# Optimization experiments

Measured on AMD Instinct MI355X. Metric: run time of the kernel, lower is better.

Reference implementation:

```python
import jax, jax.numpy as jnp
import numpy as np

# Complete binary tree: B trees, L leaves each, processed level-synchronously.
B, L, IN_DIM, MEM = 64, 1024, 300, 256


def setup_inputs() -> dict:
    key = jax.random.key(0)
    ks = jax.random.split(key, 6)
    s = 0.05
    embs = jax.random.normal(ks[0], (B, L, IN_DIM), dtype=jnp.float32)
    # Leaf module: c = cx(x); h = sigmoid(ox(x)) * tanh(c)
    Wcx = jax.random.normal(ks[1], (MEM, IN_DIM), dtype=jnp.float32) * s
    bcx = jnp.zeros((MEM,), jnp.float32)
    Wox = jax.random.normal(ks[2], (MEM, IN_DIM), dtype=jnp.float32) * s
    box = jnp.zeros((MEM,), jnp.float32)
    # Composer: 4 gates (i, lf, rf, u), each gate = Linear(lh) + Linear(rh).
    # Stacked: Wl/Wr have shape [4, MEM, MEM]; biases [4, MEM].
    Wl = jax.random.normal(ks[3], (4, MEM, MEM), dtype=jnp.float32) * s
    bl = jnp.zeros((4, MEM), jnp.float32)
    Wr = jax.random.normal(ks[4], (4, MEM, MEM), dtype=jnp.float32) * s
    br = jnp.zeros((4, MEM), jnp.float32)
    return dict(embs=embs, Wcx=Wcx, bcx=bcx, Wox=Wox, box=box,
                Wl=Wl, bl=bl, Wr=Wr, br=br)


def reference(embs, Wcx, bcx, Wox, box, Wl, bl, Wr, br):
    # Leaf module (BinaryTreeLeafModule.forward), vectorized over all leaves.
    c = jnp.einsum('blx,mx->blm', embs, Wcx) + bcx          # [B, L, MEM]
    o = jax.nn.sigmoid(jnp.einsum('blx,mx->blm', embs, Wox) + box)
    h = o * jnp.tanh(c)

    bias = bl + br                                          # [4, MEM]
    n = c.shape[1]
    while n > 1:  # log2(L) levels, static unrolled loop
        lc, rc = c[:, 0::2], c[:, 1::2]                     # [B, n/2, MEM]
        lh, rh = h[:, 0::2], h[:, 1::2]
        # All 4 gate pre-activations fused: [B, n/2, 4, MEM]
        g = (jnp.einsum('bnm,gom->bngo', lh, Wl)
             + jnp.einsum('bnm,gom->bngo', rh, Wr) + bias)
        i = jax.nn.sigmoid(g[..., 0, :])
        lf = jax.nn.sigmoid(g[..., 1, :])
        rf = jax.nn.sigmoid(g[..., 2, :])
        u = jnp.tanh(g[..., 3, :])
        c = i * u + lf * lc + rf * rc                       # composer cell
        h = jnp.tanh(c)                                     # gate_output=False path
        n //= 2

    # Root state (tree.state = (c, h)); stacked as [2, B, MEM]
    return jnp.stack([c[:, 0], h[:, 0]])
```

## Files before the change

### kernel.cpp

```cpp
#include <hip/hip_runtime.h>
#include <hip/hip_bf16.h>


typedef __attribute__((ext_vector_type(8))) short bf16x8;
typedef __attribute__((ext_vector_type(4))) float f32x4;

__device__ __forceinline__ float fsig(float x)  { return 1.f / (1.f + __expf(-x)); }
__device__ __forceinline__ float ftanh(float x) { return 1.f - 2.f / (__expf(2.f * x) + 1.f); }
__device__ __forceinline__ ushort f2bf(float x) {
    __hip_bfloat16 b = __float2bfloat16(x);
    return *reinterpret_cast<ushort*>(&b);
}

__device__ __forceinline__ void gld_lds16(const void* g, void* l) {
    __builtin_amdgcn_global_load_lds((const __attribute__((address_space(1))) void*)g,
                                     (__attribute__((address_space(3))) void*)l, 16, 0, 0);
}

__global__ void prep(const float* __restrict__ Wl,  const float* __restrict__ Wr,
                     const float* __restrict__ bl,  const float* __restrict__ br,
                     const float* __restrict__ Wcx, const float* __restrict__ Wox,
                     const float* __restrict__ bcx, const float* __restrict__ box,
                     const float* __restrict__ embs,
                     ushort* __restrict__ Wb2, ushort* __restrict__ WbL,
                     float* __restrict__ bp2, float* __restrict__ bpL,
                     ushort* __restrict__ embsB)
{
    const int gid = blockIdx.x * 256 + threadIdx.x;
    for (int i = gid; i < 524288; i += 262144) {
        int e = i & 7, slot = (i >> 3) & 3, o = (i >> 5) & 255;
        int g = (i >> 13) & 3, t = i >> 15;
        int q = slot ^ ((o >> 1) & 3);
        int k = t * 32 + q * 8 + e;
        float v = (k < 256) ? Wl[(g * 256 + o) * 256 + k]
                            : Wr[(g * 256 + o) * 256 + (k - 256)];
        Wb2[i] = f2bf(v);
    }
    if (gid < 163840) {
        int e = gid & 7, slot = (gid >> 3) & 3, o = (gid >> 5) & 255;
        int g = (gid >> 13) & 1, t = gid >> 14;
        int q = slot ^ ((o >> 1) & 3);
        int k = t * 32 + q * 8 + e;
        float v = 0.f;
        if (k < 300) v = g ? Wox[o * 300 + k] : Wcx[o * 300 + k];
        WbL[gid] = f2bf(v);
    }
    if (gid < 1024) bp2[gid] = bl[gid] + br[gid];
    if (gid < 512) {
        int g = gid >> 8, o = gid & 255;
        bpL[gid] = g ? box[o] : bcx[o];
    }
    for (int i = gid; i < 65536 * 80; i += 262144) {
        int row = i / 80;
        int k = (i - row * 80) * 4;
        float4 v = make_float4(0.f, 0.f, 0.f, 0.f);
        if (k < 300) v = *(const float4*)(embs + (size_t)row * 300 + k);
        ushort4 o4;
        o4.x = f2bf(v.x); o4.y = f2bf(v.y); o4.z = f2bf(v.z); o4.w = f2bf(v.w);
        *(ushort4*)(embsB + (size_t)row * 320 + k) = o4;
    }
}


template<int NG, int HALVES, int MODE>
__global__ __launch_bounds__(256, 3)
void mfma_gemm(const ushort* __restrict__ A,
               const ushort* __restrict__ Wb,
               const float* __restrict__ bp,
               const float* __restrict__ Cprev,
               float* __restrict__ c_out,
               ushort* __restrict__ h_out,
               int M)
{
    constexpr int K = HALVES * 32;
    constexpr int OW = 128 / NG;
    __shared__ __align__(16) ushort As[3][512 * 8];
    __shared__ __align__(16) ushort Bs[3][512 * 8];

    const int tid = threadIdx.x;
    const int wid = tid >> 6, ln = tid & 63;
    const int lq = ln >> 4, lr = ln & 15;
    const int wm = wid >> 1, wn = wid & 1;
    const int rowBlk = blockIdx.x * 128;
    const int o0 = blockIdx.y * OW;

    f32x4 acc[4][4];
#pragma unroll
    for (int m = 0; m < 4; ++m)
#pragma unroll
        for (int f = 0; f < 4; ++f) acc[m][f] = f32x4{0.f, 0.f, 0.f, 0.f};

    const int ar0 = tid >> 2,  as0 = tid & 3;
    const int ar1 = ar0 + 64;
    const int aq0 = (as0 - ((ar0 >> 1) & 3)) & 3;
    const int aq1 = (as0 - ((ar1 >> 1) & 3)) & 3;
    const ushort* aP0 = A + (size_t)min(rowBlk + ar0, M - 1) * K + aq0 * 8;
    const ushort* aP1 = A + (size_t)min(rowBlk + ar1, M - 1) * K + aq1 * 8;
    const int bj0 = tid >> 2,        bs0 = tid & 3;
    const int bj1 = (tid + 256) >> 2;
    const int bg0 = bj0 / OW, bo0 = o0 + (bj0 & (OW - 1));
    const int bg1 = bj1 / OW, bo1 = o0 + (bj1 & (OW - 1));
    const ushort* bP0 = Wb + ((size_t)bg0 * 1024 + bo0 * 4 + bs0) * 8;
    const ushort* bP1 = Wb + ((size_t)bg1 * 1024 + bo1 * 4 + bs0) * 8;
    constexpr size_t BSTR = (size_t)NG * 1024 * 8;

    const int aSw = (lq + ((lr >> 1) & 3)) & 3;
    const int bSw = lq ^ ((lr >> 1) & 3);
    int aOff[4];
#pragma unroll
    for (int m = 0; m < 4; ++m)
        aOff[m] = ((wm * 64 + m * 16 + lr) * 4 + aSw) * 8;
    int bOff[4];
#pragma unroll
    for (int f = 0; f < 4; ++f)
        bOff[f] = ((f * 32 + wn * 16 + lr) * 4 + bSw) * 8;

    gld_lds16(aP0, &As[0][tid * 8]);
    gld_lds16(aP1, &As[0][(tid + 256) * 8]);
    gld_lds16(bP0, &Bs[0][tid * 8]);
    gld_lds16(bP1, &Bs[0][(tid + 256) * 8]);
    gld_lds16(aP0 + 32, &As[1][tid * 8]);
    gld_lds16(aP1 + 32, &As[1][(tid + 256) * 8]);
    gld_lds16(bP0 + BSTR, &Bs[1][tid * 8]);
    gld_lds16(bP1 + BSTR, &Bs[1][(tid + 256) * 8]);
    asm volatile("s_waitcnt vmcnt(4)" ::: "memory");
    __builtin_amdgcn_s_barrier();
    __builtin_amdgcn_sched_barrier(0);

#pragma unroll
    for (int h = 0; h < HALVES; ++h) {
        const ushort* Ac = &As[h % 3][0];
        const ushort* Bc = &Bs[h % 3][0];
        if (h + 2 < HALVES) {
            ushort* An = &As[(h + 2) % 3][0];
            ushort* Bn = &Bs[(h + 2) % 3][0];
            gld_lds16(aP0 + (size_t)(h + 2) * 32, An + tid * 8);
            gld_lds16(aP1 + (size_t)(h + 2) * 32, An + (tid + 256) * 8);
            gld_lds16(bP0 + (size_t)(h + 2) * BSTR, Bn + tid * 8);
            gld_lds16(bP1 + (size_t)(h + 2) * BSTR, Bn + (tid + 256) * 8);
        }
        bf16x8 a[4];
#pragma unroll
        for (int m = 0; m < 4; ++m)
            a[m] = *(const bf16x8*)(Ac + aOff[m]);
#pragma unroll
        for (int f = 0; f < 4; ++f) {
            bf16x8 b = *(const bf16x8*)(Bc + bOff[f]);
#pragma unroll
            for (int m = 0; m < 4; ++m)
                acc[m][f] = __builtin_amdgcn_mfma_f32_16x16x32_bf16(a[m], b, acc[m][f], 0, 0, 0);
        }
        if (h + 1 < HALVES) {
            if (h + 2 < HALVES) asm volatile("s_waitcnt vmcnt(4)" ::: "memory");
            else                asm volatile("s_waitcnt vmcnt(0)" ::: "memory");
            __builtin_amdgcn_s_barrier();
            __builtin_amdgcn_sched_barrier(0);
        }
    }

#pragma unroll
    for (int m = 0; m < 4; ++m) {
        const int row0 = rowBlk + wm * 64 + m * 16 + lq * 4;
        if constexpr (MODE == 0) {
#pragma unroll
            for (int ob = 0; ob < 2; ++ob) {
                const int col = o0 + ob * 32 + wn * 16 + lr;
                const float bc = bp[col], bo = bp[256 + col];
#pragma unroll
                for (int j = 0; j < 4; ++j) {
                    int row = row0 + j;
                    if (row < M) {
                        float cv = acc[m][ob][j] + bc;
                        float ov = acc[m][2 + ob][j] + bo;
                        c_out[(size_t)row * 256 + col] = cv;
                        h_out[(size_t)row * 256 + col] = f2bf(fsig(ov) * ftanh(cv));
                    }
                }
            }
        } else {
            const int col = o0 + wn * 16 + lr;
            const float bi  = bp[col],       blf = bp[256 + col];
            const float brf = bp[512 + col], bu  = bp[768 + col];
#pragma unroll
            for (int j = 0; j < 4; ++j) {
                int row = row0 + j;
                if (row < M) {
                    float gi = fsig(acc[m][0][j] + bi);
                    float lf = fsig(acc[m][1][j] + blf);
                    float rf = fsig(acc[m][2][j] + brf);
                    float gu = ftanh(acc[m][3][j] + bu);
                    float lc = Cprev[(size_t)row * 512 + col];
                    float rc = Cprev[(size_t)row * 512 + 256 + col];
                    float cv = gi * gu + lf * lc + rf * rc;
                    c_out[(size_t)row * 256 + col] = cv;
                    h_out[(size_t)row * 256 + col] = f2bf(ftanh(cv));
                }
            }
        }
    }
}


__global__ __launch_bounds__(512, 1)
void tail_lstm(const ushort* __restrict__ hin,
               const float* __restrict__ cin,
               const ushort* __restrict__ Wb,
               const float* __restrict__ bp,
               float* __restrict__ dout)
{
    __shared__ __align__(16) ushort H0[64 * 256];
    __shared__ __align__(16) ushort H1[32 * 256];
    __shared__ __align__(16) float  C0[64 * 256];
    __shared__ __align__(16) float  C1[32 * 256];

    const int b = blockIdx.x;
    const int tid = threadIdx.x;
    const int wid = tid >> 6, ln = tid & 63;
    const int lq = ln >> 4, lr = ln & 15;

    for (int ct = tid; ct < 2048; ct += 512) {
        int pr = ct >> 5, pc = ct & 31;
        bf16x8 v = *(const bf16x8*)(hin + ((size_t)(b * 64 + pr) * 256 + pc * 8));
        *(bf16x8*)&H0[pr * 256 + ((pc ^ ((pr >> 1) & 7)) * 8)] = v;
    }
    for (int i = tid; i < 4096; i += 512)
        *(float4*)&C0[i * 4] = *(const float4*)(cin + (size_t)b * 64 * 256 + i * 4);
    __syncthreads();

    int o_[2], sl_[2];
    const ushort* bB[2];
#pragma unroll
    for (int of = 0; of < 2; ++of) {
        o_[of] = wid * 32 + of * 16 + lr;
        sl_[of] = lq ^ ((o_[of] >> 1) & 3);
        bB[of] = Wb + (size_t)(o_[of] * 4 + sl_[of]) * 8;
    }
    const float bi0  = bp[o_[0]],       blf0 = bp[256 + o_[0]];
    const float brf0 = bp[512 + o_[0]], bu0  = bp[768 + o_[0]];
    const float bi1  = bp[o_[1]],       blf1 = bp[256 + o_[1]];
    const float brf1 = bp[512 + o_[1]], bu1  = bp[768 + o_[1]];

    {
        f32x4 acc[2][2][4];
#pragma unroll
        for (int m = 0; m < 2; ++m)
#pragma unroll
            for (int of = 0; of < 2; ++of)
#pragma unroll
                for (int g = 0; g < 4; ++g) acc[m][of][g] = f32x4{0.f, 0.f, 0.f, 0.f};

        bf16x8 b0[2][4], b1[2][4], a0[2], a1[2];
#pragma unroll
        for (int of = 0; of < 2; ++of)
#pragma unroll
            for (int g = 0; g < 4; ++g)
                b0[of][g] = *(const bf16x8*)(bB[of] + (size_t)g * 8192);
#pragma unroll
        for (int m = 0; m < 2; ++m) {
            int pr = 32 * m + 2 * lr, pc = lq;
            a0[m] = *(const bf16x8*)&H0[pr * 256 + ((pc ^ ((pr >> 1) & 7)) * 8)];
        }

#pragma unroll 1
        for (int ks = 0; ks < 16; ks += 2) {
            if (ks + 1 < 16) {
#pragma unroll
                for (int of = 0; of < 2; ++of)
#pragma unroll
                    for (int g = 0; g < 4; ++g)
                        b1[of][g] = *(const bf16x8*)(bB[of] + (size_t)((ks + 1) * 4 + g) * 8192);
#pragma unroll
                for (int m = 0; m < 2; ++m) {
                    int pr = 32 * m + 2 * lr + ((ks + 1) >> 3), pc = lq + ((ks + 1) & 7) * 4;
                    a1[m] = *(const bf16x8*)&H0[pr * 256 + ((pc ^ ((pr >> 1) & 7)) * 8)];
                }
            }
#pragma unroll
            for (int m = 0; m < 2; ++m)
#pragma unroll
                for (int of = 0; of < 2; ++of)
#pragma unroll
                    for (int g = 0; g < 4; ++g)
                        acc[m][of][g] = __builtin_amdgcn_mfma_f32_16x16x32_bf16(a0[m], b0[of][g], acc[m][of][g], 0, 0, 0);
            if (ks + 2 < 16) {
#pragma unroll
                for (int of = 0; of < 2; ++of)
#pragma unroll
                    for (int g = 0; g < 4; ++g)
                        b0[of][g] = *(const bf16x8*)(bB[of] + (size_t)((ks + 2) * 4 + g) * 8192);
#pragma unroll
                for (int m = 0; m < 2; ++m) {
                    int pr = 32 * m + 2 * lr + ((ks + 2) >> 3), pc = lq + ((ks + 2) & 7) * 4;
                    a0[m] = *(const bf16x8*)&H0[pr * 256 + ((pc ^ ((pr >> 1) & 7)) * 8)];
                }
            }
#pragma unroll
            for (int m = 0; m < 2; ++m)
#pragma unroll
                for (int of = 0; of < 2; ++of)
#pragma unroll
                    for (int g = 0; g < 4; ++g)
                        acc[m][of][g] = __builtin_amdgcn_mfma_f32_16x16x32_bf16(a1[m], b1[of][g], acc[m][of][g], 0, 0, 0);
        }

#pragma unroll
        for (int m = 0; m < 2; ++m)
#pragma unroll
        for (int of = 0; of < 2; ++of) {
            const int col = o_[of];
            const float vbi  = of ? bi1 : bi0,   vblf = of ? blf1 : blf0;
            const float vbrf = of ? brf1 : brf0, vbu  = of ? bu1 : bu0;
#pragma unroll
            for (int j = 0; j < 4; ++j) {
                int row = m * 16 + lq * 4 + j;
                float gi = fsig(acc[m][of][0][j] + vbi);
                float lf = fsig(acc[m][of][1][j] + vblf);
                float rf = fsig(acc[m][of][2][j] + vbrf);
                float gu = ftanh(acc[m][of][3][j] + vbu);
                float lc = C0[(2 * row) * 256 + col];
                float rc = C0[(2 * row + 1) * 256 + col];
                float cv = gi * gu + lf * lc + rf * rc;
                float hv = ftanh(cv);
                C1[row * 256 + col] = cv;
                H1[row * 256 + (((col >> 3) ^ ((row >> 1) & 7)) * 8) + (col & 7)] = f2bf(hv);
            }
        }
        __syncthreads();
    }

#pragma unroll 1
    for (int lvl = 1; lvl < 6; ++lvl) {
        const int npo = 32 >> lvl;
        const ushort* Hin = (lvl & 1) ? H1 : H0;
        ushort*       Hout = (lvl & 1) ? H0 : H1;
        const float*  Cin = (lvl & 1) ? C1 : C0;
        float*        Cout = (lvl & 1) ? C0 : C1;

        f32x4 acc[2][4];
#pragma unroll
        for (int of = 0; of < 2; ++of)
#pragma unroll
            for (int g = 0; g < 4; ++g) acc[of][g] = f32x4{0.f, 0.f, 0.f, 0.f};

        bf16x8 b0[2][4], b1[2][4], a0, a1;
#pragma unroll
        for (int of = 0; of < 2; ++of)
#pragma unroll
            for (int g = 0; g < 4; ++g)
                b0[of][g] = *(const bf16x8*)(bB[of] + (size_t)g * 8192);
        {
            int pr = 2 * lr, pc = lq;
            a0 = *(const bf16x8*)&Hin[pr * 256 + ((pc ^ ((pr >> 1) & 7)) * 8)];
        }

#pragma unroll 1
        for (int ks = 0; ks < 16; ks += 2) {
            if (ks + 1 < 16) {
#pragma unroll
                for (int of = 0; of < 2; ++of)
#pragma unroll
                    for (int g = 0; g < 4; ++g)
                        b1[of][g] = *(const bf16x8*)(bB[of] + (size_t)((ks + 1) * 4 + g) * 8192);
                int pr = 2 * lr + ((ks + 1) >> 3), pc = lq + ((ks + 1) & 7) * 4;
                a1 = *(const bf16x8*)&Hin[pr * 256 + ((pc ^ ((pr >> 1) & 7)) * 8)];
            }
#pragma unroll
            for (int of = 0; of < 2; ++of)
#pragma unroll
                for (int g = 0; g < 4; ++g)
                    acc[of][g] = __builtin_amdgcn_mfma_f32_16x16x32_bf16(a0, b0[of][g], acc[of][g], 0, 0, 0);
            if (ks + 2 < 16) {
#pragma unroll
                for (int of = 0; of < 2; ++of)
#pragma unroll
                    for (int g = 0; g < 4; ++g)
                        b0[of][g] = *(const bf16x8*)(bB[of] + (size_t)((ks + 2) * 4 + g) * 8192);
                int pr = 2 * lr + ((ks + 2) >> 3), pc = lq + ((ks + 2) & 7) * 4;
                a0 = *(const bf16x8*)&Hin[pr * 256 + ((pc ^ ((pr >> 1) & 7)) * 8)];
            }
#pragma unroll
            for (int of = 0; of < 2; ++of)
#pragma unroll
                for (int g = 0; g < 4; ++g)
                    acc[of][g] = __builtin_amdgcn_mfma_f32_16x16x32_bf16(a1, b1[of][g], acc[of][g], 0, 0, 0);
        }

#pragma unroll
        for (int of = 0; of < 2; ++of) {
            const int col = o_[of];
            const float vbi  = of ? bi1 : bi0,   vblf = of ? blf1 : blf0;
            const float vbrf = of ? brf1 : brf0, vbu  = of ? bu1 : bu0;
#pragma unroll
            for (int j = 0; j < 4; ++j) {
                int row = lq * 4 + j;
                if (row < npo) {
                    float gi = fsig(acc[of][0][j] + vbi);
                    float lf = fsig(acc[of][1][j] + vblf);
                    float rf = fsig(acc[of][2][j] + vbrf);
                    float gu = ftanh(acc[of][3][j] + vbu);
                    float lc = Cin[(2 * row) * 256 + col];
                    float rc = Cin[(2 * row + 1) * 256 + col];
                    float cv = gi * gu + lf * lc + rf * rc;
                    float hv = ftanh(cv);
                    if (lvl == 5) {
                        dout[b * 256 + col] = cv;
                        dout[16384 + b * 256 + col] = hv;
                    } else {
                        Cout[row * 256 + col] = cv;
                        Hout[row * 256 + (((col >> 3) ^ ((row >> 1) & 7)) * 8) + (col & 7)] = f2bf(hv);
                    }
                }
            }
        }
        __syncthreads();
    }
}


extern "C" void kernel_launch(void* const* d_in, const int* in_sizes, int n_in,
                              void* d_out, int out_size, void* d_ws, size_t ws_size,
                              hipStream_t stream)
{
    const float* embs = (const float*)d_in[0];
    const float* Wcx  = (const float*)d_in[1];
    const float* bcx  = (const float*)d_in[2];
    const float* Wox  = (const float*)d_in[3];
    const float* box  = (const float*)d_in[4];
    const float* Wl   = (const float*)d_in[5];
    const float* bl   = (const float*)d_in[6];
    const float* Wr   = (const float*)d_in[7];
    const float* br   = (const float*)d_in[8];

    char* p = (char*)d_ws;
    ushort* Wb2 = (ushort*)p;  p += (size_t)524288 * 2;
    ushort* WbL = (ushort*)p;  p += (size_t)163840 * 2;
    float*  bp2 = (float*)p;   p += 1024 * 4;
    float*  bpL = (float*)p;   p += 512 * 4;
    float*  c0  = (float*)p;   p += (size_t)65536 * 256 * 4;
    ushort* h0  = (ushort*)p;  p += (size_t)65536 * 256 * 2;
    char* X = p;
    ushort* embsB = (ushort*)X;
    float*  cA = (float*)X;
    ushort* hA = (ushort*)(X + (size_t)32768 * 256 * 4);
    float*  cB = (float*)(X + (size_t)48 * 1024 * 1024);
    ushort* hB = (ushort*)(X + (size_t)64 * 1024 * 1024);

    prep<<<1024, 256, 0, stream>>>(Wl, Wr, bl, br, Wcx, Wox, bcx, box, embs,
                                   Wb2, WbL, bp2, bpL, embsB);

    mfma_gemm<2, 10, 0><<<dim3(512, 4), 256, 0, stream>>>(
        embsB, WbL, bpL, nullptr, c0, h0, 65536);

    mfma_gemm<4, 16, 1><<<dim3(256, 8), 256, 0, stream>>>(
        h0, Wb2, bp2, c0, cA, hA, 32768);
    mfma_gemm<4, 16, 1><<<dim3(128, 8), 256, 0, stream>>>(
        hA, Wb2, bp2, cA, cB, hB, 16384);
    mfma_gemm<4, 16, 1><<<dim3(64, 8), 256, 0, stream>>>(
        hB, Wb2, bp2, cB, cA, hA, 8192);
    mfma_gemm<4, 16, 1><<<dim3(32, 8), 256, 0, stream>>>(
        hA, Wb2, bp2, cA, cB, hB, 4096);

    tail_lstm<<<64, 512, 0, stream>>>(
        hB, cB, Wb2, bp2, (float*)d_out);
}
```

Baseline: 270.4 us.

## Store LSTM cell state in fp16 and simplify GEMM LDS pipeline

The intermediate cell-state buffers c between tree levels are now stored as fp16 instead of fp32. This halves the global memory traffic for writing and reading c in the leaf GEMM, the level GEMMs and the tail kernel, and shrinks the workspace layout. The GEMM moves from a 3-stage LDS ring with manual vmcnt waits to a 2-stage double buffer guarded by __syncthreads, and launch bounds rise to 4 blocks per CU. The tail kernel also drops its LDS staging of the first level and reads h and c straight from global memory. The risks are fp16 rounding error in c across ten levels and weaker latency hiding from the shallower prefetch.

```diff
diff --git a/kernel.cpp b/kernel.cpp
--- a/kernel.cpp
+++ b/kernel.cpp
@@ -1,5 +1,6 @@
 #include <hip/hip_runtime.h>
 #include <hip/hip_bf16.h>
+#include <hip/hip_fp16.h>
 
 
 typedef __attribute__((ext_vector_type(8))) short bf16x8;
@@ -63,19 +64,19 @@
 
 
 template<int NG, int HALVES, int MODE>
-__global__ __launch_bounds__(256, 3)
+__global__ __launch_bounds__(256, 4)
 void mfma_gemm(const ushort* __restrict__ A,
                const ushort* __restrict__ Wb,
                const float* __restrict__ bp,
-               const float* __restrict__ Cprev,
-               float* __restrict__ c_out,
+               const __half* __restrict__ Cprev,
+               __half* __restrict__ c_out,
                ushort* __restrict__ h_out,
                int M)
 {
     constexpr int K = HALVES * 32;
     constexpr int OW = 128 / NG;
-    __shared__ __align__(16) ushort As[3][512 * 8];
-    __shared__ __align__(16) ushort Bs[3][512 * 8];
+    __shared__ __align__(16) ushort As[2][512 * 8];
+    __shared__ __align__(16) ushort Bs[2][512 * 8];
 
     const int tid = threadIdx.x;
     const int wid = tid >> 6, ln = tid & 63;
@@ -119,42 +120,27 @@
     gld_lds16(aP1, &As[0][(tid + 256) * 8]);
     gld_lds16(bP0, &Bs[0][tid * 8]);
     gld_lds16(bP1, &Bs[0][(tid + 256) * 8]);
-    gld_lds16(aP0 + 32, &As[1][tid * 8]);
-    gld_lds16(aP1 + 32, &As[1][(tid + 256) * 8]);
-    gld_lds16(bP0 + BSTR, &Bs[1][tid * 8]);
-    gld_lds16(bP1 + BSTR, &Bs[1][(tid + 256) * 8]);
-    asm volatile("s_waitcnt vmcnt(4)" ::: "memory");
-    __builtin_amdgcn_s_barrier();
-    __builtin_amdgcn_sched_barrier(0);
 
 #pragma unroll
     for (int h = 0; h < HALVES; ++h) {
-        const ushort* Ac = &As[h % 3][0];
-        const ushort* Bc = &Bs[h % 3][0];
-        if (h + 2 < HALVES) {
-            ushort* An = &As[(h + 2) % 3][0];
-            ushort* Bn = &Bs[(h + 2) % 3][0];
-            gld_lds16(aP0 + (size_t)(h + 2) * 32, An + tid * 8);
-            gld_lds16(aP1 + (size_t)(h + 2) * 32, An + (tid + 256) * 8);
-            gld_lds16(bP0 + (size_t)(h + 2) * BSTR, Bn + tid * 8);
-            gld_lds16(bP1 + (size_t)(h + 2) * BSTR, Bn + (tid + 256) * 8);
+        __syncthreads();
+        const int cur = h & 1;
+        if (h + 1 < HALVES) {
+            gld_lds16(aP0 + (size_t)(h + 1) * 32, &As[cur ^ 1][tid * 8]);
+            gld_lds16(aP1 + (size_t)(h + 1) * 32, &As[cur ^ 1][(tid + 256) * 8]);
+            gld_lds16(bP0 + (size_t)(h + 1) * BSTR, &Bs[cur ^ 1][tid * 8]);
+            gld_lds16(bP1 + (size_t)(h + 1) * BSTR, &Bs[cur ^ 1][(tid + 256) * 8]);
         }
         bf16x8 a[4];
 #pragma unroll
         for (int m = 0; m < 4; ++m)
-            a[m] = *(const bf16x8*)(Ac + aOff[m]);
+            a[m] = *(const bf16x8*)&As[cur][aOff[m]];
 #pragma unroll
         for (int f = 0; f < 4; ++f) {
-            bf16x8 b = *(const bf16x8*)(Bc + bOff[f]);
+            bf16x8 b = *(const bf16x8*)&Bs[cur][bOff[f]];
 #pragma unroll
             for (int m = 0; m < 4; ++m)
                 acc[m][f] = __builtin_amdgcn_mfma_f32_16x16x32_bf16(a[m], b, acc[m][f], 0, 0, 0);
-        }
-        if (h + 1 < HALVES) {
-            if (h + 2 < HALVES) asm volatile("s_waitcnt vmcnt(4)" ::: "memory");
-            else                asm volatile("s_waitcnt vmcnt(0)" ::: "memory");
-            __builtin_amdgcn_s_barrier();
-            __builtin_amdgcn_sched_barrier(0);
         }
     }
 
@@ -172,7 +158,7 @@
                     if (row < M) {
                         float cv = acc[m][ob][j] + bc;
                         float ov = acc[m][2 + ob][j] + bo;
-                        c_out[(size_t)row * 256 + col] = cv;
+                        c_out[(size_t)row * 256 + col] = __float2half(cv);
                         h_out[(size_t)row * 256 + col] = f2bf(fsig(ov) * ftanh(cv));
                     }
                 }
@@ -189,10 +175,10 @@
                     float lf = fsig(acc[m][1][j] + blf);
                     float rf = fsig(acc[m][2][j] + brf);
                     float gu = ftanh(acc[m][3][j] + bu);
-                    float lc = Cprev[(size_t)row * 512 + col];
-                    float rc = Cprev[(size_t)row * 512 + 256 + col];
+                    float lc = __half2float(Cprev[(size_t)row * 512 + col]);
+                    float rc = __half2float(Cprev[(size_t)row * 512 + 256 + col]);
                     float cv = gi * gu + lf * lc + rf * rc;
-                    c_out[(size_t)row * 256 + col] = cv;
+                    c_out[(size_t)row * 256 + col] = __float2half(cv);
                     h_out[(size_t)row * 256 + col] = f2bf(ftanh(cv));
                 }
             }
@@ -203,30 +189,21 @@
 
 __global__ __launch_bounds__(512, 1)
 void tail_lstm(const ushort* __restrict__ hin,
-               const float* __restrict__ cin,
+               const __half* __restrict__ cin,
                const ushort* __restrict__ Wb,
                const float* __restrict__ bp,
                float* __restrict__ dout)
 {
-    __shared__ __align__(16) ushort H0[64 * 256];
-    __shared__ __align__(16) ushort H1[32 * 256];
-    __shared__ __align__(16) float  C0[64 * 256];
-    __shared__ __align__(16) float  C1[32 * 256];
+    __shared__ __align__(16) ushort HA[32 * 256];
+    __shared__ __align__(16) float  CA[32 * 256];
+    __shared__ __align__(16) ushort HB[16 * 256];
+    __shared__ __align__(16) float  CB[16 * 256];
 
     const int b = blockIdx.x;
     const int tid = threadIdx.x;
     const int wid = tid >> 6, ln = tid & 63;
     const int lq = ln >> 4, lr = ln & 15;
 
-    for (int ct = tid; ct < 2048; ct += 512) {
-        int pr = ct >> 5, pc = ct & 31;
-        bf16x8 v = *(const bf16x8*)(hin + ((size_t)(b * 64 + pr) * 256 + pc * 8));
-        *(bf16x8*)&H0[pr * 256 + ((pc ^ ((pr >> 1) & 7)) * 8)] = v;
-    }
-    for (int i = tid; i < 4096; i += 512)
-        *(float4*)&C0[i * 4] = *(const float4*)(cin + (size_t)b * 64 * 256 + i * 4);
-    __syncthreads();
-
     int o_[2], sl_[2];
     const ushort* bB[2];
 #pragma unroll
@@ -241,6 +218,7 @@
     const float brf1 = bp[512 + o_[1]], bu1  = bp[768 + o_[1]];
 
     {
+        const ushort* hbase = hin + (size_t)b * 64 * 256;
         f32x4 acc[2][2][4];
 #pragma unroll
         for (int m = 0; m < 2; ++m)
@@ -257,8 +235,8 @@
                 b0[of][g] = *(const bf16x8*)(bB[of] + (size_t)g * 8192);
 #pragma unroll
         for (int m = 0; m < 2; ++m) {
-            int pr = 32 * m + 2 * lr, pc = lq;
-            a0[m] = *(const bf16x8*)&H0[pr * 256 + ((pc ^ ((pr >> 1) & 7)) * 8)];
+            int pr = 32 * m + 2 * lr;
+            a0[m] = *(const bf16x8*)(hbase + (size_t)pr * 256 + lq * 8);
         }
 
 #pragma unroll 1
@@ -271,8 +249,9 @@
                         b1[of][g] = *(const bf16x8*)(bB[of] + (size_t)((ks + 1) * 4 + g) * 8192);
 #pragma unroll
                 for (int m = 0; m < 2; ++m) {
-                    int pr = 32 * m + 2 * lr + ((ks + 1) >> 3), pc = lq + ((ks + 1) & 7) * 4;
-                    a1[m] = *(const bf16x8*)&H0[pr * 256 + ((pc ^ ((pr >> 1) & 7)) * 8)];
+                    int pr = 32 * m + 2 * lr + ((ks + 1) >> 3);
+                    int pc = lq + ((ks + 1) & 7) * 4;
+                    a1[m] = *(const bf16x8*)(hbase + (size_t)pr * 256 + pc * 8);
                 }
             }
 #pragma unroll
@@ -290,8 +269,9 @@
                         b0[of][g] = *(const bf16x8*)(bB[of] + (size_t)((ks + 2) * 4 + g) * 8192);
 #pragma unroll
                 for (int m = 0; m < 2; ++m) {
-                    int pr = 32 * m + 2 * lr + ((ks + 2) >> 3), pc = lq + ((ks + 2) & 7) * 4;
-                    a0[m] = *(const bf16x8*)&H0[pr * 256 + ((pc ^ ((pr >> 1) & 7)) * 8)];
+                    int pr = 32 * m + 2 * lr + ((ks + 2) >> 3);
+                    int pc = lq + ((ks + 2) & 7) * 4;
+                    a0[m] = *(const bf16x8*)(hbase + (size_t)pr * 256 + pc * 8);
                 }
             }
 #pragma unroll
@@ -303,6 +283,7 @@
                         acc[m][of][g] = __builtin_amdgcn_mfma_f32_16x16x32_bf16(a1[m], b1[of][g], acc[m][of][g], 0, 0, 0);
         }
 
+        const __half* cbase = cin + (size_t)b * 64 * 256;
 #pragma unroll
         for (int m = 0; m < 2; ++m)
 #pragma unroll
@@ -317,12 +298,12 @@
                 float lf = fsig(acc[m][of][1][j] + vblf);
                 float rf = fsig(acc[m][of][2][j] + vbrf);
                 float gu = ftanh(acc[m][of][3][j] + vbu);
-                float lc = C0[(2 * row) * 256 + col];
-                float rc = C0[(2 * row + 1) * 256 + col];
+                float lc = __half2float(cbase[(size_t)(2 * row) * 256 + col]);
+                float rc = __half2float(cbase[(size_t)(2 * row + 1) * 256 + col]);
                 float cv = gi * gu + lf * lc + rf * rc;
                 float hv = ftanh(cv);
-                C1[row * 256 + col] = cv;
-                H1[row * 256 + (((col >> 3) ^ ((row >> 1) & 7)) * 8) + (col & 7)] = f2bf(hv);
+                CA[row * 256 + col] = cv;
+                HA[row * 256 + (((col >> 3) ^ ((row >> 1) & 7)) * 8) + (col & 7)] = f2bf(hv);
             }
         }
         __syncthreads();
@@ -331,10 +312,10 @@
 #pragma unroll 1
     for (int lvl = 1; lvl < 6; ++lvl) {
         const int npo = 32 >> lvl;
-        const ushort* Hin = (lvl & 1) ? H1 : H0;
-        ushort*       Hout = (lvl & 1) ? H0 : H1;
-        const float*  Cin = (lvl & 1) ? C1 : C0;
-        float*        Cout = (lvl & 1) ? C0 : C1;
+        const ushort* Hin = (lvl & 1) ? HA : HB;
+        ushort*       Hout = (lvl & 1) ? HB : HA;
+        const float*  Cin = (lvl & 1) ? CA : CB;
+        float*        Cout = (lvl & 1) ? CB : CA;
 
         f32x4 acc[2][4];
 #pragma unroll
@@ -349,8 +330,8 @@
             for (int g = 0; g < 4; ++g)
                 b0[of][g] = *(const bf16x8*)(bB[of] + (size_t)g * 8192);
         {
-            int pr = 2 * lr, pc = lq;
-            a0 = *(const bf16x8*)&Hin[pr * 256 + ((pc ^ ((pr >> 1) & 7)) * 8)];
+            int pr = 2 * lr;
+            a0 = *(const bf16x8*)&Hin[pr * 256 + ((lq ^ ((pr >> 1) & 7)) * 8)];
         }
 
 #pragma unroll 1
@@ -436,14 +417,14 @@
     ushort* WbL = (ushort*)p;  p += (size_t)163840 * 2;
     float*  bp2 = (float*)p;   p += 1024 * 4;
     float*  bpL = (float*)p;   p += 512 * 4;
-    float*  c0  = (float*)p;   p += (size_t)65536 * 256 * 4;
+    __half* c0  = (__half*)p;  p += (size_t)65536 * 256 * 2;
     ushort* h0  = (ushort*)p;  p += (size_t)65536 * 256 * 2;
     char* X = p;
     ushort* embsB = (ushort*)X;
-    float*  cA = (float*)X;
-    ushort* hA = (ushort*)(X + (size_t)32768 * 256 * 4);
-    float*  cB = (float*)(X + (size_t)48 * 1024 * 1024);
-    ushort* hB = (ushort*)(X + (size_t)64 * 1024 * 1024);
+    __half* cA = (__half*)X;
+    ushort* hA = (ushort*)(X + (size_t)16 * 1024 * 1024);
+    __half* cB = (__half*)(X + (size_t)32 * 1024 * 1024);
+    ushort* hB = (ushort*)(X + (size_t)40 * 1024 * 1024);
 
     prep<<<1024, 256, 0, stream>>>(Wl, Wr, bl, br, Wcx, Wox, bcx, box, embs,
                                    Wb2, WbL, bp2, bpL, embsB);
```

New measurement: 257.4 us. 4.8% less time.
